# Optimization experiments

Measured on AMD Instinct MI355X. Metric: run time of the kernel, lower is better.

## Reference

```python
import jax, jax.numpy as jnp
import numpy as np

H = 1024
W = 1024
SAMPLES_PER_SEG = 32
SIGMA_AA = 1.0
EDGE_CHUNK = 32  # matches torch chunk_size


def sample_bezier_path(control_points):
    # control_points: [N, 2], N = 3*S + 1 cubic segments
    N = control_points.shape[0]
    S = (N - 1) // 3
    idx = 3 * jnp.arange(S)
    p0 = control_points[idx][:, None, :]      # [S,1,2]
    p1 = control_points[idx + 1][:, None, :]
    p2 = control_points[idx + 2][:, None, :]
    p3 = control_points[idx + 3][:, None, :]
    t = jnp.linspace(0.0, 1.0, SAMPLES_PER_SEG, dtype=control_points.dtype)[None, :, None]  # [1,T,1]
    mt = 1.0 - t
    pts = (mt * mt * mt) * p0 + 3.0 * (mt * mt) * t * p1 + 3.0 * mt * (t * t) * p2 + (t * t * t) * p3
    return pts.reshape(S * SAMPLES_PER_SEG, 2)  # [M,2]


def compute_winding(path_points, sigma):
    # path_points: [M,2]; closed polygon edges (j -> (j+1)%M)
    M = path_points.shape[0]
    nxt = jnp.roll(path_points, -1, axis=0)
    x0, y0 = path_points[:, 0], path_points[:, 1]
    x1, y1 = nxt[:, 0], nxt[:, 1]
    dy = y1 - y0
    dx = x1 - x0
    # edges with |dy| < 1e-6 are skipped in the original (continue) -> zero contribution
    coeff = jnp.sign(dy) * (jnp.abs(dy) >= 1e-6).astype(path_points.dtype)
    grid_y = jnp.arange(H, dtype=path_points.dtype)  # rows
    grid_x = jnp.arange(W, dtype=path_points.dtype)  # cols

    n_chunks = M // EDGE_CHUNK
    def chunk_it(a):
        return a.reshape(n_chunks, EDGE_CHUNK)

    def body(acc, c):
        cx0, cy0, cdy, cdx, cc = c  # each [CH]
        t_cross = (grid_y[None, :] - cy0[:, None]) / (cdy[:, None] + 1e-8)          # [CH,H]
        x_cross = cx0[:, None] + t_cross * cdx[:, None]                              # [CH,H]
        valid_t = jax.nn.sigmoid(t_cross * 20.0) * jax.nn.sigmoid((1.0 - t_cross) * 20.0)  # [CH,H]
        crosses = jax.nn.sigmoid((x_cross[:, :, None] - grid_x[None, None, :]) / sigma)    # [CH,H,W]
        contrib = jnp.sum(crosses * (valid_t * cc[:, None])[:, :, None], axis=0)           # [H,W]
        return acc + contrib, None

    init = jnp.zeros((H, W), dtype=path_points.dtype)
    winding, _ = jax.lax.scan(body, init, (chunk_it(x0), chunk_it(y0), chunk_it(dy), chunk_it(dx), chunk_it(coeff)))
    return winding


def setup_inputs() -> dict:
    key = jax.random.key(0)
    k1, k2 = jax.random.split(key)
    control_points = jax.random.uniform(k1, (49, 2), dtype=jnp.float32) * jnp.float32(W)
    color = jax.random.uniform(k2, (3,), dtype=jnp.float32)
    return {"control_points": control_points, "color": color}


def reference(control_points, color):
    pts = sample_bezier_path(control_points)          # [M,2]
    winding = compute_winding(pts, SIGMA_AA)          # [H,W]
    alpha = jax.nn.sigmoid(winding * 4.0)             # [H,W]
    rgb = jnp.broadcast_to(color[None, None, :], (H, W, 3))
    rgba = jnp.concatenate([rgb, alpha[..., None]], axis=-1)  # [H,W,4]
    return rgba
```

## Files before the change

kernel.cpp:

```cpp
#include <hip/hip_runtime.h>

#define HH 1024
#define WW 1024
#define NPTS 512
#define W_EPS 1e-6f
#define CAP 64

__device__ __forceinline__ float sigmoidf(float z) {
    float e = __expf(-z);
    return __builtin_amdgcn_rcpf(1.0f + e);
}

__global__ __launch_bounds__(256) void render_kernel(
    const float* __restrict__ cp,
    const float* __restrict__ color,
    float* __restrict__ out)
{
    __shared__ float2 pts[NPTS];
    __shared__ float2 actXW[NPTS];
    __shared__ int    actTmin[NPTS];
    __shared__ int    actTmax[NPTS];
    __shared__ float2 bucket[16][CAP];
    __shared__ int    cnt[16];
    __shared__ float  satW[16];
    __shared__ int    n_act;

    const int tid = threadIdx.x;
    const int y = blockIdx.x;
    const float yf = (float)y;

    if (tid == 0) n_act = 0;
    if (tid < 16) cnt[tid] = 0;

    for (int i = tid; i < NPTS; i += 256) {
        int seg = i >> 5;
        int j = i & 31;
        float t = (float)j / 31.0f;
        float mt = 1.0f - t;
        int bb = 3 * seg * 2;
        float p0x = cp[bb + 0], p0y = cp[bb + 1];
        float p1x = cp[bb + 2], p1y = cp[bb + 3];
        float p2x = cp[bb + 4], p2y = cp[bb + 5];
        float p3x = cp[bb + 6], p3y = cp[bb + 7];
        float a0 = mt * mt * mt;
        float a1 = 3.0f * mt * mt * t;
        float a2 = 3.0f * mt * t * t;
        float a3 = t * t * t;
        pts[i] = make_float2(a0 * p0x + a1 * p1x + a2 * p2x + a3 * p3x,
                             a0 * p0y + a1 * p1y + a2 * p2y + a3 * p3y);
    }
    __syncthreads();

    for (int e = tid; e < NPTS; e += 256) {
        float2 p = pts[e];
        float2 q = pts[(e + 1) & (NPTS - 1)];
        float dy = q.y - p.y;
        float dx = q.x - p.x;
        float c = (dy > 0.0f) ? 1.0f : ((dy < 0.0f) ? -1.0f : 0.0f);
        if (fabsf(dy) < 1e-6f) c = 0.0f;
        float t = (yf - p.y) / (dy + 1e-8f);
        float vt = sigmoidf(t * 20.0f) * sigmoidf((1.0f - t) * 20.0f);
        float w = vt * c;
        if (fabsf(w) > W_EPS) {
            float xc = p.x + t * dx;
            int tmin = (int)ceilf((xc - 77.0f) * 0.015625f);
            if (tmin < 0) tmin = 0;
            if (tmin > 16) tmin = 16;
            int tmax = (int)floorf((xc + 14.0f) * 0.015625f);
            if (tmax > 15) tmax = 15;
            int idx = atomicAdd(&n_act, 1);
            actXW[idx] = make_float2(xc, w);
            actTmin[idx] = tmin;
            actTmax[idx] = tmax;
            for (int tt = tmin; tt <= tmax; ++tt) {
                int pos = atomicAdd(&cnt[tt], 1);
                if (pos < CAP) bucket[tt][pos] = make_float2(xc, w);
            }
        }
    }
    __syncthreads();

    const int n = n_act;

    {
        int grp = tid >> 4;
        int l16 = tid & 15;
        float partial = 0.0f;
        for (int i = l16; i < n; i += 16)
            if (grp < actTmin[i]) partial += actXW[i].y;
        partial += __shfl_down(partial, 8, 16);
        partial += __shfl_down(partial, 4, 16);
        partial += __shfl_down(partial, 2, 16);
        partial += __shfl_down(partial, 1, 16);
        if (l16 == 0) satW[grp] = partial;
    }
    __syncthreads();

    const float cr = color[0], cg = color[1], cb = color[2];
    const int wv = tid >> 6;
    const int lane = tid & 63;
    float4* orow = ((float4*)out) + y * WW;

    for (int k = 0; k < 4; ++k) {
        const int t = k * 4 + wv;
        const int x = t * 64 + lane;
        const float xf = (float)x;
        float acc;
        const int m = cnt[t];
        if (m <= CAP) {
            acc = satW[t];
            for (int j = 0; j < m; ++j) {
                float2 d = bucket[t][j];
                acc = fmaf(d.y, sigmoidf(d.x - xf), acc);
            }
        } else {
            acc = 0.0f;
            for (int i = 0; i < n; ++i) {
                int tmin = actTmin[i];
                if (t < tmin) {
                    acc += actXW[i].y;
                } else if (t <= actTmax[i]) {
                    float2 d = actXW[i];
                    acc = fmaf(d.y, sigmoidf(d.x - xf), acc);
                }
            }
        }
        orow[x] = make_float4(cr, cg, cb, sigmoidf(4.0f * acc));
    }
}

extern "C" void kernel_launch(void* const* d_in, const int* in_sizes, int n_in,
                              void* d_out, int out_size, void* d_ws, size_t ws_size,
                              hipStream_t stream) {
    const float* cp = (const float*)d_in[0];
    const float* color = (const float*)d_in[1];
    float* out = (float*)d_out;
    render_kernel<<<HH, 256, 0, stream>>>(cp, color, out);
}
```

Measured before the change: 64.44 us.

## Process two rows per block sharing Bezier sampling, and early-reject edges

Each 512-thread block now handles two image rows, with each half owning its own shared-memory row context, so the Bezier point sampling is computed once per pair of rows instead of once per row. Edge processing also adds a cheap t-range test before computing the sigmoids, which skips edges whose crossing parameter is far outside [0,1]. The cost is doubled shared-memory use per block, which may lower occupancy, and the early rejection treats edges with t outside (-0.7, 1.7) as contributing nothing.

```diff
diff --git a/kernel.cpp b/kernel.cpp
--- a/kernel.cpp
+++ b/kernel.cpp
@@ -11,28 +11,35 @@
     return __builtin_amdgcn_rcpf(1.0f + e);
 }
 
-__global__ __launch_bounds__(256) void render_kernel(
+struct RowCtx {
+    float2 actXW[NPTS];
+    int    actTmin[NPTS];
+    int    actTmax[NPTS];
+    float2 bucket[16][CAP];
+    int    cnt[16];
+    float  satW[16];
+    int    n_act;
+};
+
+__global__ __launch_bounds__(512) void render_kernel(
     const float* __restrict__ cp,
     const float* __restrict__ color,
     float* __restrict__ out)
 {
     __shared__ float2 pts[NPTS];
-    __shared__ float2 actXW[NPTS];
-    __shared__ int    actTmin[NPTS];
-    __shared__ int    actTmax[NPTS];
-    __shared__ float2 bucket[16][CAP];
-    __shared__ int    cnt[16];
-    __shared__ float  satW[16];
-    __shared__ int    n_act;
+    __shared__ RowCtx rc[2];
 
-    const int tid = threadIdx.x;
-    const int y = blockIdx.x;
+    const int tid  = threadIdx.x;
+    const int half = tid >> 8;
+    const int htid = tid & 255;
+    const int y    = (blockIdx.x << 1) + half;
     const float yf = (float)y;
 
-    if (tid == 0) n_act = 0;
-    if (tid < 16) cnt[tid] = 0;
+    if (htid == 0) rc[half].n_act = 0;
+    if (htid < 16) rc[half].cnt[htid] = 0;
 
-    for (int i = tid; i < NPTS; i += 256) {
+    {
+        const int i = tid;
         int seg = i >> 5;
         int j = i & 31;
         float t = (float)j / 31.0f;
@@ -51,53 +58,57 @@
     }
     __syncthreads();
 
-    for (int e = tid; e < NPTS; e += 256) {
+    for (int e = htid; e < NPTS; e += 256) {
         float2 p = pts[e];
         float2 q = pts[(e + 1) & (NPTS - 1)];
         float dy = q.y - p.y;
-        float dx = q.x - p.x;
-        float c = (dy > 0.0f) ? 1.0f : ((dy < 0.0f) ? -1.0f : 0.0f);
-        if (fabsf(dy) < 1e-6f) c = 0.0f;
         float t = (yf - p.y) / (dy + 1e-8f);
-        float vt = sigmoidf(t * 20.0f) * sigmoidf((1.0f - t) * 20.0f);
-        float w = vt * c;
-        if (fabsf(w) > W_EPS) {
-            float xc = p.x + t * dx;
-            int tmin = (int)ceilf((xc - 77.0f) * 0.015625f);
-            if (tmin < 0) tmin = 0;
-            if (tmin > 16) tmin = 16;
-            int tmax = (int)floorf((xc + 14.0f) * 0.015625f);
-            if (tmax > 15) tmax = 15;
-            int idx = atomicAdd(&n_act, 1);
-            actXW[idx] = make_float2(xc, w);
-            actTmin[idx] = tmin;
-            actTmax[idx] = tmax;
-            for (int tt = tmin; tt <= tmax; ++tt) {
-                int pos = atomicAdd(&cnt[tt], 1);
-                if (pos < CAP) bucket[tt][pos] = make_float2(xc, w);
+        if (t > -0.70f && t < 1.70f) {
+            float c = (dy > 0.0f) ? 1.0f : ((dy < 0.0f) ? -1.0f : 0.0f);
+            if (fabsf(dy) < 1e-6f) c = 0.0f;
+            if (c != 0.0f) {
+                float vt = sigmoidf(t * 20.0f) * sigmoidf((1.0f - t) * 20.0f);
+                float w = vt * c;
+                if (fabsf(w) > W_EPS) {
+                    float dx = q.x - p.x;
+                    float xc = p.x + t * dx;
+                    int tmin = (int)ceilf((xc - 77.0f) * 0.015625f);
+                    if (tmin < 0) tmin = 0;
+                    if (tmin > 16) tmin = 16;
+                    int tmax = (int)floorf((xc + 14.0f) * 0.015625f);
+                    if (tmax > 15) tmax = 15;
+                    int idx = atomicAdd(&rc[half].n_act, 1);
+                    rc[half].actXW[idx] = make_float2(xc, w);
+                    rc[half].actTmin[idx] = tmin;
+                    rc[half].actTmax[idx] = tmax;
+                    for (int tt = tmin; tt <= tmax; ++tt) {
+                        int pos = atomicAdd(&rc[half].cnt[tt], 1);
+                        if (pos < CAP) rc[half].bucket[tt][pos] = make_float2(xc, w);
+                    }
+                }
             }
         }
     }
     __syncthreads();
 
-    const int n = n_act;
+    const int n = rc[half].n_act;
 
     {
-        int grp = tid >> 4;
-        int l16 = tid & 15;
+        int grp = htid >> 4;
+        int l16 = htid & 15;
         float partial = 0.0f;
         for (int i = l16; i < n; i += 16)
-            if (grp < actTmin[i]) partial += actXW[i].y;
+            if (grp < rc[half].actTmin[i]) partial += rc[half].actXW[i].y;
         partial += __shfl_down(partial, 8, 16);
         partial += __shfl_down(partial, 4, 16);
         partial += __shfl_down(partial, 2, 16);
         partial += __shfl_down(partial, 1, 16);
-        if (l16 == 0) satW[grp] = partial;
+        if (l16 == 0) rc[half].satW[grp] = partial;
     }
     __syncthreads();
 
     const float cr = color[0], cg = color[1], cb = color[2];
-    const int wv = tid >> 6;
+    const int wv = (tid >> 6) & 3;
     const int lane = tid & 63;
     float4* orow = ((float4*)out) + y * WW;
 
@@ -106,21 +117,21 @@
         const int x = t * 64 + lane;
         const float xf = (float)x;
         float acc;
-        const int m = cnt[t];
+        const int m = rc[half].cnt[t];
         if (m <= CAP) {
-            acc = satW[t];
+            acc = rc[half].satW[t];
             for (int j = 0; j < m; ++j) {
-                float2 d = bucket[t][j];
+                float2 d = rc[half].bucket[t][j];
                 acc = fmaf(d.y, sigmoidf(d.x - xf), acc);
             }
         } else {
             acc = 0.0f;
             for (int i = 0; i < n; ++i) {
-                int tmin = actTmin[i];
+                int tmin = rc[half].actTmin[i];
                 if (t < tmin) {
-                    acc += actXW[i].y;
-                } else if (t <= actTmax[i]) {
-                    float2 d = actXW[i];
+                    acc += rc[half].actXW[i].y;
+                } else if (t <= rc[half].actTmax[i]) {
+                    float2 d = rc[half].actXW[i];
                     acc = fmaf(d.y, sigmoidf(d.x - xf), acc);
                 }
             }
@@ -135,5 +146,5 @@
     const float* cp = (const float*)d_in[0];
     const float* color = (const float*)d_in[1];
     float* out = (float*)d_out;
-    render_kernel<<<HH, 256, 0, stream>>>(cp, color, out);
+    render_kernel<<<HH / 2, 512, 0, stream>>>(cp, color, out);
 }
```

Result: no change. 64.73 us (+0.5%).
